# Performance work log

Hardware: AMD Instinct MI355X
Metric: run time of the kernel (lower is better)

## Reference

```python
import jax, jax.numpy as jnp
import numpy as np


def setup_inputs() -> dict:
    key = jax.random.key(0)
    B, D = 8192, 4096
    ks = jax.random.split(key, 6)
    s = 1.0 / np.sqrt(D)  # nn.init.uniform_(-1/sqrt(D), 1/sqrt(D))
    return {
        "u": jax.random.normal(ks[0], (B, D), dtype=jnp.float32),
        "w1": jax.random.uniform(ks[1], (D,), jnp.float32, -s, s),
        "w2": jax.random.uniform(ks[2], (D,), jnp.float32, -s, s),
        "w3": jax.random.uniform(ks[3], (D,), jnp.float32, -s, s),
        "bias1": jnp.ones((1,), jnp.float32),
        "bias2": jnp.ones((1,), jnp.float32),
        # nn.Linear(D, 1): kaiming-uniform-ish init approximated with same bound
        "delta_w": jax.random.uniform(ks[4], (1, D), jnp.float32, -s, s),
        "delta_b": jax.random.uniform(ks[5], (1,), jnp.float32, -s, s),
    }


def reference(u, w1, w2, w3, bias1, bias2, delta_w, delta_b):
    # select = softplus(delta(u) + bias1), shape [B]
    select = jax.nn.softplus(u @ delta_w.T + delta_b + bias1)[:, 0]
    # einsum('bi,b->b', M, x) == (sum_i M[b,i]) * x[b], so the recurrence
    # collapses to scalar-per-batch coefficients:
    a = select * (u @ w1)   # sum_i Abar[b,i] = select[b] * sum_i w1[i]*u[b,i]
    b = u @ w2              # sum_i Bbar[b,i]
    c = u @ w3              # sum_i Cbar[b,i]
    Dc = bias2[0]
    ut = u.T                # [T, B], time-major for scan; T == input_dim
    x0 = b * ut[0]          # xi at step 0; y[:,0] = x0 (no C/D term in original)

    def step(x, ui):
        xn = a * x + b * ui
        return xn, c * xn + Dc * ui

    _, ys = jax.lax.scan(step, x0, ut[1:])  # ys: [T-1, B]
    y = jnp.concatenate([x0[None, :], ys], axis=0).T  # [B, T]
    return y
```

## Files before the change

### kernel.cpp

```cpp
#include <hip/hip_runtime.h>
#include <hip/hip_bf16.h>
#include <math.h>


#define DDIM 4096

__device__ inline float softplus_ref(float z) {
    return (z > 0.0f) ? (z + log1pf(expf(-z))) : log1pf(expf(z));
}

__device__ inline float finitize(double v) {
    long long b   = __double_as_longlong(v);
    long long mag = b & 0x7FFFFFFFFFFFFFFFLL;
    if (mag > 0x7FF0000000000000LL) return 0.0f;
    const long long LIM = 0x47D8479E7CEA1E6ALL;
    float f;
    if (mag >= LIM) f = 3.3e38f;
    else            f = (float)v;
    return (b < 0) ? -f : f;
}

__device__ inline double shfl_up_d(double x, int delta) {
    int lo = __double2loint(x);
    int hi = __double2hiint(x);
    lo = __shfl_up(lo, delta, 64);
    hi = __shfl_up(hi, delta, 64);
    return __hiloint2double(hi, lo);
}

__device__ inline double shfl_d(double x, int src) {
    int lo = __double2loint(x);
    int hi = __double2hiint(x);
    lo = __shfl(lo, src, 64);
    hi = __shfl(hi, src, 64);
    return __hiloint2double(hi, lo);
}

__global__ __launch_bounds__(256) void ssm_kernel(
    const float* __restrict__ u,
    const float* __restrict__ w1,
    const float* __restrict__ w2,
    const float* __restrict__ w3,
    const float* __restrict__ bias1,
    const float* __restrict__ bias2,
    const float* __restrict__ dw,
    const float* __restrict__ db,
    float* __restrict__ y)
{
    const int wid  = threadIdx.x >> 6;
    const int lane = threadIdx.x & 63;
    const int row  = (blockIdx.x << 2) + wid;

    const float* __restrict__ urow = u + (size_t)row * DDIM;
    float* __restrict__ yrow       = y + (size_t)row * DDIM;

    float s0 = 0.f, s1 = 0.f, s2 = 0.f, s3 = 0.f;
#pragma unroll 4
    for (int c = 0; c < DDIM / 256; ++c) {
        const int idx = c * 256 + lane * 4;
        const float4 uv = *reinterpret_cast<const float4*>(urow + idx);
        const float4 dv = *reinterpret_cast<const float4*>(dw + idx);
        const float4 a1 = *reinterpret_cast<const float4*>(w1 + idx);
        const float4 a2 = *reinterpret_cast<const float4*>(w2 + idx);
        const float4 a3 = *reinterpret_cast<const float4*>(w3 + idx);
        s0 += uv.x * dv.x + uv.y * dv.y + uv.z * dv.z + uv.w * dv.w;
        s1 += uv.x * a1.x + uv.y * a1.y + uv.z * a1.z + uv.w * a1.w;
        s2 += uv.x * a2.x + uv.y * a2.y + uv.z * a2.z + uv.w * a2.w;
        s3 += uv.x * a3.x + uv.y * a3.y + uv.z * a3.z + uv.w * a3.w;
    }
#pragma unroll
    for (int d = 1; d < 64; d <<= 1) {
        s0 += __shfl_xor(s0, d, 64);
        s1 += __shfl_xor(s1, d, 64);
        s2 += __shfl_xor(s2, d, 64);
        s3 += __shfl_xor(s3, d, 64);
    }

    const float sel = softplus_ref(s0 + db[0] + bias1[0]);
    const float af  = sel * s1;

    const double ad  = (double)af;
    const double bbd = (double)s2;
    const double ccd = (double)s3;
    const double Dcd = (double)bias2[0];

    double r1 = ad * ad; r1 = r1 * r1;
    const double r2  = r1 * r1;
    const double r4  = r2 * r2;
    const double r8  = r4 * r4;
    const double r16 = r8 * r8;
    const double r32 = r16 * r16;
    double P = 1.0;
    if (lane & 1)  P *= r1;
    if (lane & 2)  P *= r2;
    if (lane & 4)  P *= r4;
    if (lane & 8)  P *= r8;
    if (lane & 16) P *= r16;
    if (lane & 32) P *= r32;

    double x_in = 0.0;
    for (int c = 0; c < DDIM / 256; ++c) {
        const int idx = c * 256 + lane * 4;
        const float4 uv = *reinterpret_cast<const float4*>(urow + idx);
        const double v0 = bbd * (double)uv.x;
        const double v1 = bbd * (double)uv.y;
        const double v2 = bbd * (double)uv.z;
        const double v3 = bbd * (double)uv.w;

        double B = v0;
        B = fma(ad, B, v1);
        B = fma(ad, B, v2);
        B = fma(ad, B, v3);

        double Bp;
        Bp = shfl_up_d(B, 1);  if (lane >= 1)  B = fma(r1,  Bp, B);
        Bp = shfl_up_d(B, 2);  if (lane >= 2)  B = fma(r2,  Bp, B);
        Bp = shfl_up_d(B, 4);  if (lane >= 4)  B = fma(r4,  Bp, B);
        Bp = shfl_up_d(B, 8);  if (lane >= 8)  B = fma(r8,  Bp, B);
        Bp = shfl_up_d(B, 16); if (lane >= 16) B = fma(r16, Bp, B);
        Bp = shfl_up_d(B, 32); if (lane >= 32) B = fma(r32, Bp, B);

        double Cprev = shfl_up_d(B, 1);
        if (lane == 0) Cprev = 0.0;

        const double x_start = fma(P, x_in, Cprev);
        const double x0 = fma(ad, x_start, v0);
        const double x1 = fma(ad, x0, v1);
        const double x2 = fma(ad, x1, v2);
        const double x3 = fma(ad, x2, v3);

        float4 yv;
        yv.x = finitize(fma(ccd, x0, Dcd * (double)uv.x));
        yv.y = finitize(fma(ccd, x1, Dcd * (double)uv.y));
        yv.z = finitize(fma(ccd, x2, Dcd * (double)uv.z));
        yv.w = finitize(fma(ccd, x3, Dcd * (double)uv.w));
        if (c == 0 && lane == 0) yv.x = finitize(x0);
        *reinterpret_cast<float4*>(yrow + idx) = yv;

        x_in = shfl_d(x3, 63);
    }
}

extern "C" void kernel_launch(void* const* d_in, const int* in_sizes, int n_in,
                              void* d_out, int out_size, void* d_ws, size_t ws_size,
                              hipStream_t stream) {
    const float* u     = (const float*)d_in[0];
    const float* w1    = (const float*)d_in[1];
    const float* w2    = (const float*)d_in[2];
    const float* w3    = (const float*)d_in[3];
    const float* bias1 = (const float*)d_in[4];
    const float* bias2 = (const float*)d_in[5];
    const float* dw    = (const float*)d_in[6];
    const float* db    = (const float*)d_in[7];
    float* y = (float*)d_out;

    const int B = in_sizes[0] / DDIM;
    dim3 grid(B / 4), block(256);
    hipLaunchKernelGGL(ssm_kernel, grid, block, 0, stream,
                       u, w1, w2, w3, bias1, bias2, dw, db, y);
}
```

Measured before the change: 273.6 us.

## Switch scan to fp32 with register-cached row and decoupled chunk carries

Moves the per-row linear recurrence from double to float arithmetic and clamps values with a cheap bit-mask instead of the double finitize routine. The u row is kept in registers (16 float4 per lane), so the second global read of the row goes away. The 16 per-chunk warp prefix scans are computed independently before the sequential pass, and the carry is chained through a precomputed a^256 factor, so the shuffle chains are off the serial dependency path. The risks are reduced precision against the double-based reference, and higher register pressure, which may lower occupancy.

```diff
diff --git a/kernel.cpp b/kernel.cpp
--- a/kernel.cpp
+++ b/kernel.cpp
@@ -1,39 +1,20 @@
 #include <hip/hip_runtime.h>
-#include <hip/hip_bf16.h>
 #include <math.h>
 
 
 #define DDIM 4096
+#define NCH  16
 
-__device__ inline float softplus_ref(float z) {
-    return (z > 0.0f) ? (z + log1pf(expf(-z))) : log1pf(expf(z));
+__device__ __forceinline__ float clf(float v) {
+    int b   = __float_as_int(v);
+    int mag = b & 0x7fffffff;
+    if (mag >= 0x7F7A0000)
+        v = __int_as_float((b & 0x80000000) | 0x7F7A0000);
+    return v;
 }
 
-__device__ inline float finitize(double v) {
-    long long b   = __double_as_longlong(v);
-    long long mag = b & 0x7FFFFFFFFFFFFFFFLL;
-    if (mag > 0x7FF0000000000000LL) return 0.0f;
-    const long long LIM = 0x47D8479E7CEA1E6ALL;
-    float f;
-    if (mag >= LIM) f = 3.3e38f;
-    else            f = (float)v;
-    return (b < 0) ? -f : f;
-}
-
-__device__ inline double shfl_up_d(double x, int delta) {
-    int lo = __double2loint(x);
-    int hi = __double2hiint(x);
-    lo = __shfl_up(lo, delta, 64);
-    hi = __shfl_up(hi, delta, 64);
-    return __hiloint2double(hi, lo);
-}
-
-__device__ inline double shfl_d(double x, int src) {
-    int lo = __double2loint(x);
-    int hi = __double2hiint(x);
-    lo = __shfl(lo, src, 64);
-    hi = __shfl(hi, src, 64);
-    return __hiloint2double(hi, lo);
+__device__ __forceinline__ float softplus_ref(float z) {
+    return (z > 0.0f) ? (z + log1pf(expf(-z))) : log1pf(expf(z));
 }
 
 __global__ __launch_bounds__(256) void ssm_kernel(
@@ -54,19 +35,20 @@
     const float* __restrict__ urow = u + (size_t)row * DDIM;
     float* __restrict__ yrow       = y + (size_t)row * DDIM;
 
+    float4 uv[NCH];
     float s0 = 0.f, s1 = 0.f, s2 = 0.f, s3 = 0.f;
-#pragma unroll 4
-    for (int c = 0; c < DDIM / 256; ++c) {
+#pragma unroll
+    for (int c = 0; c < NCH; ++c) {
         const int idx = c * 256 + lane * 4;
-        const float4 uv = *reinterpret_cast<const float4*>(urow + idx);
+        uv[c] = *reinterpret_cast<const float4*>(urow + idx);
         const float4 dv = *reinterpret_cast<const float4*>(dw + idx);
         const float4 a1 = *reinterpret_cast<const float4*>(w1 + idx);
         const float4 a2 = *reinterpret_cast<const float4*>(w2 + idx);
         const float4 a3 = *reinterpret_cast<const float4*>(w3 + idx);
-        s0 += uv.x * dv.x + uv.y * dv.y + uv.z * dv.z + uv.w * dv.w;
-        s1 += uv.x * a1.x + uv.y * a1.y + uv.z * a1.z + uv.w * a1.w;
-        s2 += uv.x * a2.x + uv.y * a2.y + uv.z * a2.z + uv.w * a2.w;
-        s3 += uv.x * a3.x + uv.y * a3.y + uv.z * a3.z + uv.w * a3.w;
+        s0 += uv[c].x * dv.x + uv[c].y * dv.y + uv[c].z * dv.z + uv[c].w * dv.w;
+        s1 += uv[c].x * a1.x + uv[c].y * a1.y + uv[c].z * a1.z + uv[c].w * a1.w;
+        s2 += uv[c].x * a2.x + uv[c].y * a2.y + uv[c].z * a2.z + uv[c].w * a2.w;
+        s3 += uv[c].x * a3.x + uv[c].y * a3.y + uv[c].z * a3.z + uv[c].w * a3.w;
     }
 #pragma unroll
     for (int d = 1; d < 64; d <<= 1) {
@@ -77,67 +59,73 @@
     }
 
     const float sel = softplus_ref(s0 + db[0] + bias1[0]);
-    const float af  = sel * s1;
+    const float a   = clf(sel * s1);
+    const float bb  = s2;
+    const float cc  = s3;
+    const float Dc  = bias2[0];
 
-    const double ad  = (double)af;
-    const double bbd = (double)s2;
-    const double ccd = (double)s3;
-    const double Dcd = (double)bias2[0];
+    const float a2p  = clf(a * a);
+    const float r1   = clf(a2p * a2p);
+    const float r2   = clf(r1 * r1);
+    const float r4   = clf(r2 * r2);
+    const float r8   = clf(r4 * r4);
+    const float r16  = clf(r8 * r8);
+    const float r32  = clf(r16 * r16);
+    const float a256 = clf(r32 * r32);
+    float P = 1.0f;
+    if (lane & 1)  P = clf(P * r1);
+    if (lane & 2)  P = clf(P * r2);
+    if (lane & 4)  P = clf(P * r4);
+    if (lane & 8)  P = clf(P * r8);
+    if (lane & 16) P = clf(P * r16);
+    if (lane & 32) P = clf(P * r32);
 
-    double r1 = ad * ad; r1 = r1 * r1;
-    const double r2  = r1 * r1;
-    const double r4  = r2 * r2;
-    const double r8  = r4 * r4;
-    const double r16 = r8 * r8;
-    const double r32 = r16 * r16;
-    double P = 1.0;
-    if (lane & 1)  P *= r1;
-    if (lane & 2)  P *= r2;
-    if (lane & 4)  P *= r4;
-    if (lane & 8)  P *= r8;
-    if (lane & 16) P *= r16;
-    if (lane & 32) P *= r32;
+    float Bv[NCH];
+#pragma unroll
+    for (int c = 0; c < NCH; ++c) {
+        float B = bb * uv[c].x;
+        B = fmaf(a, B, bb * uv[c].y);
+        B = fmaf(a, B, bb * uv[c].z);
+        B = fmaf(a, B, bb * uv[c].w);
+        Bv[c] = clf(B);
+    }
 
-    double x_in = 0.0;
-    for (int c = 0; c < DDIM / 256; ++c) {
+#pragma unroll
+    for (int c = 0; c < NCH; ++c) {
+        float B = Bv[c];
+        float t;
+        t = __shfl_up(B, 1,  64); if (lane >= 1)  B = clf(fmaf(r1,  t, B));
+        t = __shfl_up(B, 2,  64); if (lane >= 2)  B = clf(fmaf(r2,  t, B));
+        t = __shfl_up(B, 4,  64); if (lane >= 4)  B = clf(fmaf(r4,  t, B));
+        t = __shfl_up(B, 8,  64); if (lane >= 8)  B = clf(fmaf(r8,  t, B));
+        t = __shfl_up(B, 16, 64); if (lane >= 16) B = clf(fmaf(r16, t, B));
+        t = __shfl_up(B, 32, 64); if (lane >= 32) B = clf(fmaf(r32, t, B));
+        Bv[c] = B;
+    }
+
+    float cr = 0.0f;
+#pragma unroll
+    for (int c = 0; c < NCH; ++c) {
         const int idx = c * 256 + lane * 4;
-        const float4 uv = *reinterpret_cast<const float4*>(urow + idx);
-        const double v0 = bbd * (double)uv.x;
-        const double v1 = bbd * (double)uv.y;
-        const double v2 = bbd * (double)uv.z;
-        const double v3 = bbd * (double)uv.w;
+        const float T = __shfl(Bv[c], 63, 64);
+        float Cprev   = __shfl_up(Bv[c], 1, 64);
+        if (lane == 0) Cprev = 0.0f;
 
-        double B = v0;
-        B = fma(ad, B, v1);
-        B = fma(ad, B, v2);
-        B = fma(ad, B, v3);
-
-        double Bp;
-        Bp = shfl_up_d(B, 1);  if (lane >= 1)  B = fma(r1,  Bp, B);
-        Bp = shfl_up_d(B, 2);  if (lane >= 2)  B = fma(r2,  Bp, B);
-        Bp = shfl_up_d(B, 4);  if (lane >= 4)  B = fma(r4,  Bp, B);
-        Bp = shfl_up_d(B, 8);  if (lane >= 8)  B = fma(r8,  Bp, B);
-        Bp = shfl_up_d(B, 16); if (lane >= 16) B = fma(r16, Bp, B);
-        Bp = shfl_up_d(B, 32); if (lane >= 32) B = fma(r32, Bp, B);
-
-        double Cprev = shfl_up_d(B, 1);
-        if (lane == 0) Cprev = 0.0;
-
-        const double x_start = fma(P, x_in, Cprev);
-        const double x0 = fma(ad, x_start, v0);
-        const double x1 = fma(ad, x0, v1);
-        const double x2 = fma(ad, x1, v2);
-        const double x3 = fma(ad, x2, v3);
+        const float xs = clf(fmaf(P, cr, Cprev));
+        const float x0 = clf(fmaf(a, xs, bb * uv[c].x));
+        const float x1 = clf(fmaf(a, x0, bb * uv[c].y));
+        const float x2 = clf(fmaf(a, x1, bb * uv[c].z));
+        const float x3 = clf(fmaf(a, x2, bb * uv[c].w));
 
         float4 yv;
-        yv.x = finitize(fma(ccd, x0, Dcd * (double)uv.x));
-        yv.y = finitize(fma(ccd, x1, Dcd * (double)uv.y));
-        yv.z = finitize(fma(ccd, x2, Dcd * (double)uv.z));
-        yv.w = finitize(fma(ccd, x3, Dcd * (double)uv.w));
-        if (c == 0 && lane == 0) yv.x = finitize(x0);
+        yv.x = clf(fmaf(cc, x0, Dc * uv[c].x));
+        yv.y = clf(fmaf(cc, x1, Dc * uv[c].y));
+        yv.z = clf(fmaf(cc, x2, Dc * uv[c].z));
+        yv.w = clf(fmaf(cc, x3, Dc * uv[c].w));
+        if (c == 0 && lane == 0) yv.x = x0;
         *reinterpret_cast<float4*>(yrow + idx) = yv;
 
-        x_in = shfl_d(x3, 63);
+        cr = clf(fmaf(a256, cr, T));
     }
 }
 
```

Result: faster. 251.3 us (-8.2%).
